# Optimization experiments

Hardware: AMD Instinct MI355X
Metric: run time of the kernel (lower is better)

## Reference

```python
import jax, jax.numpy as jnp
import numpy as np

B, S, D_IN, D_HEAD = 8, 2048, 1024, 128
DROPOUT_RATE = 0.2


def setup_inputs() -> dict:
    key = jax.random.key(0)
    k_in, k_q, k_k, k_v, k_bq, k_bk, k_bv, k_drop = jax.random.split(key, 8)
    bound = 1.0 / np.sqrt(D_IN)  # torch nn.Linear default init range
    inp = {
        "input": jax.random.normal(k_in, (B, S, D_IN), dtype=jnp.float32),
        # weights stored [in, out] so y = x @ W + b (== torch x @ W_t.T + b)
        "Wq": jax.random.uniform(k_q, (D_IN, D_HEAD), jnp.float32, -bound, bound),
        "bq": jax.random.uniform(k_bq, (D_HEAD,), jnp.float32, -bound, bound),
        "Wk": jax.random.uniform(k_k, (D_IN, D_HEAD), jnp.float32, -bound, bound),
        "bk": jax.random.uniform(k_bk, (D_HEAD,), jnp.float32, -bound, bound),
        "Wv": jax.random.uniform(k_v, (D_IN, D_HEAD), jnp.float32, -bound, bound),
        "bv": jax.random.uniform(k_bv, (D_HEAD,), jnp.float32, -bound, bound),
        # deterministic inverted-dropout mask: 0 with prob p, else 1/(1-p)
        "drop_mask": (jax.random.uniform(k_drop, (B, S, S)) >= DROPOUT_RATE).astype(jnp.float32) / (1.0 - DROPOUT_RATE),
    }
    return inp


def reference(input, Wq, bq, Wk, bk, Wv, bv, drop_mask):
    # projections: [B, S, H]
    Q = input @ Wq + bq
    K = input @ Wk + bk
    V = input @ Wv + bv
    # raw scores, NO 1/sqrt(d) scaling (faithful to source)
    wei = jnp.einsum("bsh,bth->bst", Q, K)  # [B, S, S]
    causal = jnp.tril(jnp.ones((S, S), dtype=bool))
    wei = jnp.where(causal, wei, 0.0)  # torch.tril zeros the upper triangle
    # source sets EVERY exact zero (masked upper triangle + accidental zeros) to -inf
    wei = jnp.where(wei == 0.0, -jnp.inf, wei)
    attn = jax.nn.softmax(wei, axis=-1)
    attn = attn * drop_mask  # dropout
    return jnp.einsum("bst,bth->bsh", attn, V)
```

## Files before the change

kernel.cpp:

```cpp
#include <hip/hip_runtime.h>
#include <cstdint>
#include <cmath>

#define DEV static __device__ __forceinline__

typedef __attribute__((ext_vector_type(8))) short bf16x8;
typedef __attribute__((ext_vector_type(4))) float f32x4;

constexpr int B_  = 8;
constexpr int S_  = 2048;
constexpr int DIN = 1024;
constexpr int DH  = 128;
constexpr int M_  = B_ * S_;

DEV uint16_t bf16_rne(float f) {
  uint32_t u = __float_as_uint(f);
  u += 0x7FFFu + ((u >> 16) & 1u);
  return (uint16_t)(u >> 16);
}
DEV float bf16_f32(uint16_t h) { return __uint_as_float(((uint32_t)h) << 16); }
DEV void split2(float f, uint16_t& h, uint16_t& l) {
  h = bf16_rne(f);
  l = bf16_rne(f - bf16_f32(h));
}
DEV f32x4 mfma(bf16x8 a, bf16x8 b, f32x4 c) {
  return __builtin_amdgcn_mfma_f32_16x16x32_bf16(a, b, c, 0, 0, 0);
}
DEV bf16x8 ld8(const uint16_t* p) { return *reinterpret_cast<const bf16x8*>(p); }
DEV void gload_lds16(const uint16_t* g, uint16_t* l) {
  __builtin_amdgcn_global_load_lds(
      (const __attribute__((address_space(1))) void*)g,
      (__attribute__((address_space(3))) void*)l, 16, 0, 0);
}

__global__ __launch_bounds__(256) void k_split_x(const float* __restrict__ src,
                                                 uint16_t* __restrict__ hi,
                                                 uint16_t* __restrict__ lo, int n4) {
  int i = blockIdx.x * 256 + threadIdx.x;
  const int stride = gridDim.x * 256;
  for (; i < n4; i += stride) {
    float4 v = reinterpret_cast<const float4*>(src)[i];
    ushort4 h4, l4; uint16_t h, l;
    split2(v.x, h, l); h4.x = h; l4.x = l;
    split2(v.y, h, l); h4.y = h; l4.y = l;
    split2(v.z, h, l); h4.z = h; l4.z = l;
    split2(v.w, h, l); h4.w = h; l4.w = l;
    reinterpret_cast<ushort4*>(hi)[i] = h4;
    reinterpret_cast<ushort4*>(lo)[i] = l4;
  }
}

__global__ __launch_bounds__(256) void k_mask_bits(const float* __restrict__ m,
                                                   unsigned long long* __restrict__ bits,
                                                   int n) {
  int i = blockIdx.x * 256 + threadIdx.x;
  const int stride = gridDim.x * 256;
  for (; i < n; i += stride) {
    const int srow = (i >> 11) & (S_ - 1);
    const int col  = i & (S_ - 1);
    if ((col & ~63) <= srow) {
      const unsigned long long b = __ballot(m[i] != 0.0f);
      if ((threadIdx.x & 63) == 0) bits[i >> 6] = b;
    }
  }
}

__global__ __launch_bounds__(256) void k_split_wt(const float* __restrict__ w0,
                                                  const float* __restrict__ w1,
                                                  const float* __restrict__ w2,
                                                  uint16_t* __restrict__ thi,
                                                  uint16_t* __restrict__ tlo) {
  const int pj = blockIdx.y;
  const float* w = pj == 0 ? w0 : (pj == 1 ? w1 : w2);
  const int idx = blockIdx.x * 256 + threadIdx.x;
  const int d = idx / DIN, k = idx % DIN;
  float f = w[k * DH + d];
  uint16_t h, l;
  split2(f, h, l);
  thi[(size_t)pj * DH * DIN + idx] = h;
  tlo[(size_t)pj * DH * DIN + idx] = l;
}

__global__ __launch_bounds__(256) void k_proj(
    const uint16_t* __restrict__ xhi, const uint16_t* __restrict__ xlo,
    const uint16_t* __restrict__ wthi, const uint16_t* __restrict__ wtlo,
    const float* __restrict__ bq, const float* __restrict__ bk, const float* __restrict__ bv,
    uint16_t* __restrict__ qhi, uint16_t* __restrict__ qlo,
    uint16_t* __restrict__ khi, uint16_t* __restrict__ klo,
    uint16_t* __restrict__ vt) {
  __shared__ uint16_t As_hi[128][64], As_lo[128][64];
  __shared__ uint16_t Bs_hi[64][64],  Bs_lo[64][64];
  const int sblk = blockIdx.x;
  const int proj = blockIdx.y;
  const uint16_t* Whi = wthi + (size_t)proj * (DH * DIN);
  const uint16_t* Wlo = wtlo + (size_t)proj * (DH * DIN);

  const int tid = threadIdx.x;
  const int wid = tid >> 6, lane = tid & 63;
  const int g = lane >> 4, c16 = lane & 15;
  const int wr = wid >> 1, wc = wid & 1;

  f32x4 acc[4][2] = {};

  auto STAGE = [&](int k0) {
#pragma unroll
    for (int i = 0; i < 4; ++i) {
      const int c = tid + i * 256;
      const int row = c >> 3, sl = c & 7;
      const int col = (sl ^ (row & 7)) * 8;
      const uint32_t so = (uint32_t)row * DIN + k0 + col;
      gload_lds16(Whi + so, &As_hi[0][0] + c * 8);
      gload_lds16(Wlo + so, &As_lo[0][0] + c * 8);
    }
#pragma unroll
    for (int i = 0; i < 2; ++i) {
      const int c = tid + i * 256;
      const int row = c >> 3, sl = c & 7;
      const int col = (sl ^ (row & 7)) * 8;
      const uint32_t so = (uint32_t)(sblk * 64 + row) * DIN + k0 + col;
      gload_lds16(xhi + so, &Bs_hi[0][0] + c * 8);
      gload_lds16(xlo + so, &Bs_lo[0][0] + c * 8);
    }
  };
  auto COMPUTE = [&]() {
#pragma unroll
    for (int kk = 0; kk < 2; ++kk) {
      bf16x8 AH[4], AL[4], BH[2], BL[2];
#pragma unroll
      for (int mf = 0; mf < 4; ++mf) {
        const int row = wr * 64 + mf * 16 + c16;
        const int col = ((g + kk * 4) ^ (row & 7)) * 8;
        AH[mf] = ld8(&As_hi[row][col]);
        AL[mf] = ld8(&As_lo[row][col]);
      }
#pragma unroll
      for (int nf = 0; nf < 2; ++nf) {
        const int row = wc * 32 + nf * 16 + c16;
        const int col = ((g + kk * 4) ^ (row & 7)) * 8;
        BH[nf] = ld8(&Bs_hi[row][col]);
        BL[nf] = ld8(&Bs_lo[row][col]);
      }
#pragma unroll
      for (int mf = 0; mf < 4; ++mf)
#pragma unroll
        for (int nf = 0; nf < 2; ++nf) {
          acc[mf][nf] = mfma(AH[mf], BH[nf], acc[mf][nf]);
          acc[mf][nf] = mfma(AH[mf], BL[nf], acc[mf][nf]);
          acc[mf][nf] = mfma(AL[mf], BH[nf], acc[mf][nf]);
        }
    }
  };

  for (int k0 = 0; k0 < DIN; k0 += 64) {
    __syncthreads();
    STAGE(k0);
    __syncthreads();
    COMPUTE();
  }

  if (proj < 2) {
    const float* bias = (proj == 0) ? bq : bk;
    uint16_t* ohi = (proj == 0) ? qhi : khi;
    uint16_t* olo = (proj == 0) ? qlo : klo;
#pragma unroll
    for (int mf = 0; mf < 4; ++mf) {
      const int d0 = wr * 64 + mf * 16 + g * 4;
      const float4 bs = *reinterpret_cast<const float4*>(bias + d0);
#pragma unroll
      for (int nf = 0; nf < 2; ++nf) {
        const int srow = sblk * 64 + wc * 32 + nf * 16 + c16;
        f32x4 v = acc[mf][nf];
        ushort4 h4, l4; uint16_t h, l;
        split2(v[0] + bs.x, h, l); h4.x = h; l4.x = l;
        split2(v[1] + bs.y, h, l); h4.y = h; l4.y = l;
        split2(v[2] + bs.z, h, l); h4.z = h; l4.z = l;
        split2(v[3] + bs.w, h, l); h4.w = h; l4.w = l;
        *reinterpret_cast<ushort4*>(ohi + (size_t)srow * DH + d0) = h4;
        *reinterpret_cast<ushort4*>(olo + (size_t)srow * DH + d0) = l4;
      }
    }
  } else {
#pragma unroll
    for (int mf = 0; mf < 4; ++mf) {
      const int d0 = wr * 64 + mf * 16 + g * 4;
      const float4 bs = *reinterpret_cast<const float4*>(bv + d0);
#pragma unroll
      for (int nf = 0; nf < 2; ++nf) {
        const int srow = sblk * 64 + wc * 32 + nf * 16 + c16;
        const int b = srow >> 11;
        const int sin = srow & (S_ - 1);
        f32x4 v = acc[mf][nf];
        vt[((size_t)b * DH + d0 + 0) * S_ + sin] = bf16_rne(v[0] + bs.x);
        vt[((size_t)b * DH + d0 + 1) * S_ + sin] = bf16_rne(v[1] + bs.y);
        vt[((size_t)b * DH + d0 + 2) * S_ + sin] = bf16_rne(v[2] + bs.z);
        vt[((size_t)b * DH + d0 + 3) * S_ + sin] = bf16_rne(v[3] + bs.w);
      }
    }
  }
}

__global__ __launch_bounds__(256) void k_attn(
    const uint16_t* __restrict__ qhi, const uint16_t* __restrict__ qlo,
    const uint16_t* __restrict__ khi, const uint16_t* __restrict__ klo,
    const uint16_t* __restrict__ vt,
    const unsigned long long* __restrict__ bits,
    float* __restrict__ out) {
  __shared__ uint16_t plds[4][16][72];
  const int tid = threadIdx.x;
  const int wid = tid >> 6, lane = tid & 63;
  const int g = lane >> 4, c16 = lane & 15;
  const int unit = blockIdx.x * 4 + wid;
  const int b = unit >> 7;
  const int uu = unit & 127;
  const int qt = (uu & 1) ? (127 - (uu >> 1)) : (uu >> 1);
  const int q0 = qt * 16;
  const int qrow = q0 + c16;

  const uint32_t qoff = (uint32_t)(b * S_ + qrow) * DH + g * 8;
  bf16x8 qH[4], qL[4];
#pragma unroll
  for (int c2 = 0; c2 < 4; ++c2) {
    qH[c2] = ld8(qhi + qoff + c2 * 32);
    qL[c2] = ld8(qlo + qoff + c2 * 32);
  }

  f32x4 acc[8] = {};
  float m_run = -1e30f, l_run = 0.0f;
  const int ntile = (q0 + 16 + 63) >> 6;
  const uint32_t brow = (uint32_t)(b * S_ + qrow) * (S_ / 64);

  for (int t = 0; t < ntile; ++t) {
    const int j0 = t * 64;
    const unsigned long long bw = bits[brow + t];
    f32x4 st[4] = {};
#pragma unroll
    for (int kf = 0; kf < 4; ++kf) {
      const uint32_t koff = (uint32_t)(b * S_ + j0 + kf * 16 + c16) * DH + g * 8;
#pragma unroll
      for (int c2 = 0; c2 < 4; ++c2) {
        const bf16x8 kH = ld8(khi + koff + c2 * 32);
        const bf16x8 kL = ld8(klo + koff + c2 * 32);
        st[kf] = mfma(kH, qH[c2], st[kf]);
        st[kf] = mfma(kH, qL[c2], st[kf]);
        st[kf] = mfma(kL, qH[c2], st[kf]);
      }
    }
    float tmax = -INFINITY;
#pragma unroll
    for (int kf = 0; kf < 4; ++kf)
#pragma unroll
      for (int r = 0; r < 4; ++r) {
        const int kg = j0 + kf * 16 + g * 4 + r;
        float s = st[kf][r];
        s = (kg <= qrow && s != 0.0f) ? s : -INFINITY;
        st[kf][r] = s;
        tmax = fmaxf(tmax, s);
      }
    tmax = fmaxf(tmax, __shfl_xor(tmax, 16));
    tmax = fmaxf(tmax, __shfl_xor(tmax, 32));
    const float m_new = fmaxf(m_run, tmax);
    const float fs = __expf(m_run - m_new);
    m_run = m_new;
    float psum = 0.0f;
#pragma unroll
    for (int kf = 0; kf < 4; ++kf)
#pragma unroll
      for (int r = 0; r < 4; ++r) {
        const float pv = __expf(st[kf][r] - m_new);
        psum += pv;
        st[kf][r] = pv;
      }
    l_run = l_run * fs + psum;
#pragma unroll
    for (int kf = 0; kf < 4; ++kf) {
      const int bi = kf * 16 + g * 4;
      ushort4 pb;
      pb.x = bf16_rne(((bw >> (bi + 0)) & 1ull) ? st[kf][0] * 1.25f : 0.0f);
      pb.y = bf16_rne(((bw >> (bi + 1)) & 1ull) ? st[kf][1] * 1.25f : 0.0f);
      pb.z = bf16_rne(((bw >> (bi + 2)) & 1ull) ? st[kf][2] * 1.25f : 0.0f);
      pb.w = bf16_rne(((bw >> (bi + 3)) & 1ull) ? st[kf][3] * 1.25f : 0.0f);
      *reinterpret_cast<ushort4*>(&plds[wid][c16][kf * 16 + g * 4]) = pb;
    }
#pragma unroll
    for (int mf = 0; mf < 8; ++mf) acc[mf] *= fs;
#pragma unroll
    for (int kc = 0; kc < 2; ++kc) {
      const bf16x8 pB = *reinterpret_cast<const bf16x8*>(&plds[wid][c16][kc * 32 + g * 8]);
#pragma unroll
      for (int mf = 0; mf < 8; ++mf) {
        const uint32_t voff = (uint32_t)(b * DH + mf * 16 + c16) * S_ + j0 + kc * 32 + g * 8;
        acc[mf] = mfma(ld8(vt + voff), pB, acc[mf]);
      }
    }
  }
  l_run += __shfl_xor(l_run, 16);
  l_run += __shfl_xor(l_run, 32);
  const float inv = 1.0f / l_run;
  const uint32_t orow = (uint32_t)(b * S_ + qrow) * DH;
#pragma unroll
  for (int mf = 0; mf < 8; ++mf) {
    float4 o;
    o.x = acc[mf][0] * inv;
    o.y = acc[mf][1] * inv;
    o.z = acc[mf][2] * inv;
    o.w = acc[mf][3] * inv;
    *reinterpret_cast<float4*>(out + orow + mf * 16 + g * 4) = o;
  }
}

extern "C" void kernel_launch(void* const* d_in, const int* in_sizes, int n_in,
                              void* d_out, int out_size, void* d_ws, size_t ws_size,
                              hipStream_t stream) {
  const float* x    = (const float*)d_in[0];
  const float* Wq   = (const float*)d_in[1];
  const float* bq   = (const float*)d_in[2];
  const float* Wk   = (const float*)d_in[3];
  const float* bk   = (const float*)d_in[4];
  const float* Wv   = (const float*)d_in[5];
  const float* bv   = (const float*)d_in[6];
  const float* mask = (const float*)d_in[7];
  float* out = (float*)d_out;

  char* p = (char*)d_ws;
  auto take = [&](size_t bytes) {
    char* r = p;
    p += (bytes + 255) & ~(size_t)255;
    return r;
  };
  uint16_t* xhi  = (uint16_t*)take((size_t)M_ * DIN * 2);
  uint16_t* xlo  = (uint16_t*)take((size_t)M_ * DIN * 2);
  uint16_t* wthi = (uint16_t*)take((size_t)3 * DH * DIN * 2);
  uint16_t* wtlo = (uint16_t*)take((size_t)3 * DH * DIN * 2);
  uint16_t* qhi  = (uint16_t*)take((size_t)M_ * DH * 2);
  uint16_t* qlo  = (uint16_t*)take((size_t)M_ * DH * 2);
  uint16_t* khi  = (uint16_t*)take((size_t)M_ * DH * 2);
  uint16_t* klo  = (uint16_t*)take((size_t)M_ * DH * 2);
  uint16_t* vt   = (uint16_t*)take((size_t)M_ * DH * 2);
  unsigned long long* bits = (unsigned long long*)take((size_t)B_ * S_ * S_ / 8);

  k_split_x<<<2048, 256, 0, stream>>>(x, xhi, xlo, M_ * DIN / 4);
  k_mask_bits<<<2048, 256, 0, stream>>>(mask, bits, B_ * S_ * S_);
  k_split_wt<<<dim3(DH * DIN / 256, 3), 256, 0, stream>>>(Wq, Wk, Wv, wthi, wtlo);
  k_proj<<<dim3(M_ / 64, 3), 256, 0, stream>>>(xhi, xlo, wthi, wtlo, bq, bk, bv,
                                               qhi, qlo, khi, klo, vt);
  k_attn<<<(B_ * S_ / 16) / 4, 256, 0, stream>>>(qhi, qlo, khi, klo, vt, bits, out);
}
```

Before: 442.6 us.

## Stage K/V tiles in double-buffered swizzled LDS shared across block waves

The attention kernel now has each block cover 64 contiguous query rows, one 16-row slice per wave, so all four waves share the same K and V tiles. Those tiles are loaded into double-buffered, XOR-swizzled shared memory with direct global-to-LDS loads, prefetching the next tile while the current one is computed. This is meant to cut redundant global/L2 traffic and overlap loads with MFMA work. The cost is about 80KB of LDS per block, which lowers occupancy, and the grid shrinks to 256 blocks with less balanced causal work per block.

```diff
diff --git a/kernel.cpp b/kernel.cpp
--- a/kernel.cpp
+++ b/kernel.cpp
@@ -205,16 +205,18 @@
     const uint16_t* __restrict__ vt,
     const unsigned long long* __restrict__ bits,
     float* __restrict__ out) {
+  __shared__ uint16_t Ks_hi[2][64][128];
+  __shared__ uint16_t Ks_lo[2][64][128];
+  __shared__ uint16_t Vs[2][128][64];
   __shared__ uint16_t plds[4][16][72];
   const int tid = threadIdx.x;
   const int wid = tid >> 6, lane = tid & 63;
   const int g = lane >> 4, c16 = lane & 15;
-  const int unit = blockIdx.x * 4 + wid;
-  const int b = unit >> 7;
-  const int uu = unit & 127;
-  const int qt = (uu & 1) ? (127 - (uu >> 1)) : (uu >> 1);
-  const int q0 = qt * 16;
+  const int b  = blockIdx.x & 7;
+  const int gq = 31 - (blockIdx.x >> 3);
+  const int q0 = gq * 64 + wid * 16;
   const int qrow = q0 + c16;
+  const int nt = gq + 1;
 
   const uint32_t qoff = (uint32_t)(b * S_ + qrow) * DH + g * 8;
   bf16x8 qH[4], qL[4];
@@ -226,20 +228,46 @@
 
   f32x4 acc[8] = {};
   float m_run = -1e30f, l_run = 0.0f;
-  const int ntile = (q0 + 16 + 63) >> 6;
   const uint32_t brow = (uint32_t)(b * S_ + qrow) * (S_ / 64);
 
-  for (int t = 0; t < ntile; ++t) {
+  auto STAGE = [&](int t, int bi) {
+    const int j0 = t * 64;
+#pragma unroll
+    for (int i = 0; i < 4; ++i) {
+      const int c = tid + i * 256;
+      const int r = c >> 4, p = c & 15;
+      const int q = (p & 8) | ((p ^ r) & 7);
+      const uint32_t so = (uint32_t)(b * S_ + j0 + r) * DH + q * 8;
+      gload_lds16(khi + so, &Ks_hi[bi][0][0] + c * 8);
+      gload_lds16(klo + so, &Ks_lo[bi][0][0] + c * 8);
+    }
+#pragma unroll
+    for (int i = 0; i < 4; ++i) {
+      const int c = tid + i * 256;
+      const int r = c >> 3, p = c & 7;
+      const int q = p ^ (r & 7);
+      const uint32_t so = (uint32_t)(b * DH + r) * S_ + j0 + q * 8;
+      gload_lds16(vt + so, &Vs[bi][0][0] + c * 8);
+    }
+  };
+
+  STAGE(0, 0);
+  for (int t = 0; t < nt; ++t) {
+    __syncthreads();
+    if (t + 1 < nt) STAGE(t + 1, (t + 1) & 1);
+    const int bi = t & 1;
     const int j0 = t * 64;
     const unsigned long long bw = bits[brow + t];
     f32x4 st[4] = {};
 #pragma unroll
     for (int kf = 0; kf < 4; ++kf) {
-      const uint32_t koff = (uint32_t)(b * S_ + j0 + kf * 16 + c16) * DH + g * 8;
+      const int r = kf * 16 + c16;
 #pragma unroll
       for (int c2 = 0; c2 < 4; ++c2) {
-        const bf16x8 kH = ld8(khi + koff + c2 * 32);
-        const bf16x8 kL = ld8(klo + koff + c2 * 32);
+        const int q = g + 4 * c2;
+        const int p = (q & 8) | ((q ^ (r & 7)) & 7);
+        const bf16x8 kH = ld8(&Ks_hi[bi][r][p * 8]);
+        const bf16x8 kL = ld8(&Ks_lo[bi][r][p * 8]);
         st[kf] = mfma(kH, qH[c2], st[kf]);
         st[kf] = mfma(kH, qL[c2], st[kf]);
         st[kf] = mfma(kL, qH[c2], st[kf]);
@@ -273,12 +301,12 @@
     l_run = l_run * fs + psum;
 #pragma unroll
     for (int kf = 0; kf < 4; ++kf) {
-      const int bi = kf * 16 + g * 4;
+      const int bi2 = kf * 16 + g * 4;
       ushort4 pb;
-      pb.x = bf16_rne(((bw >> (bi + 0)) & 1ull) ? st[kf][0] * 1.25f : 0.0f);
-      pb.y = bf16_rne(((bw >> (bi + 1)) & 1ull) ? st[kf][1] * 1.25f : 0.0f);
-      pb.z = bf16_rne(((bw >> (bi + 2)) & 1ull) ? st[kf][2] * 1.25f : 0.0f);
-      pb.w = bf16_rne(((bw >> (bi + 3)) & 1ull) ? st[kf][3] * 1.25f : 0.0f);
+      pb.x = bf16_rne(((bw >> (bi2 + 0)) & 1ull) ? st[kf][0] * 1.25f : 0.0f);
+      pb.y = bf16_rne(((bw >> (bi2 + 1)) & 1ull) ? st[kf][1] * 1.25f : 0.0f);
+      pb.z = bf16_rne(((bw >> (bi2 + 2)) & 1ull) ? st[kf][2] * 1.25f : 0.0f);
+      pb.w = bf16_rne(((bw >> (bi2 + 3)) & 1ull) ? st[kf][3] * 1.25f : 0.0f);
       *reinterpret_cast<ushort4*>(&plds[wid][c16][kf * 16 + g * 4]) = pb;
     }
 #pragma unroll
@@ -288,8 +316,10 @@
       const bf16x8 pB = *reinterpret_cast<const bf16x8*>(&plds[wid][c16][kc * 32 + g * 8]);
 #pragma unroll
       for (int mf = 0; mf < 8; ++mf) {
-        const uint32_t voff = (uint32_t)(b * DH + mf * 16 + c16) * S_ + j0 + kc * 32 + g * 8;
-        acc[mf] = mfma(ld8(vt + voff), pB, acc[mf]);
+        const int r = mf * 16 + c16;
+        const int q = kc * 4 + g;
+        const int p = q ^ (r & 7);
+        acc[mf] = mfma(ld8(&Vs[bi][r][p * 8]), pB, acc[mf]);
       }
     }
   }
@@ -343,5 +373,5 @@
   k_split_wt<<<dim3(DH * DIN / 256, 3), 256, 0, stream>>>(Wq, Wk, Wv, wthi, wtlo);
   k_proj<<<dim3(M_ / 64, 3), 256, 0, stream>>>(xhi, xlo, wthi, wtlo, bq, bk, bv,
                                                qhi, qlo, khi, klo, vt);
-  k_attn<<<(B_ * S_ / 16) / 4, 256, 0, stream>>>(qhi, qlo, khi, klo, vt, bits, out);
-}
+  k_attn<<<256, 256, 0, stream>>>(qhi, qlo, khi, klo, vt, bits, out);
+}
```

Measured after the change: 392.4 us. 11.4% less time.
